# Optimization experiments

Hardware: AMD Instinct MI355X
Metric: run time of the kernel (lower is better)

Reference implementation:

```python
import jax, jax.numpy as jnp
import numpy as np

B, T, D, U = 64, 128, 1024, 1024


def setup_inputs() -> dict:
    key = jax.random.key(0)
    k_x, k_r, k_s, k_wi, k_wh = jax.random.split(key, 5)
    x = jax.random.normal(k_x, (B, T, D), dtype=jnp.float32)
    reset = jax.random.randint(k_r, (B, T), 0, 2, dtype=jnp.int32)
    state = jax.random.normal(k_s, (B, T, U), dtype=jnp.float32)
    # hk.GRU params: w_i (input->3*hidden), w_h (hidden->3*hidden), bias (3*hidden)
    w_i = jax.random.normal(k_wi, (D, 3 * U), dtype=jnp.float32) * (1.0 / np.sqrt(D))
    w_h = jax.random.normal(k_wh, (U, 3 * U), dtype=jnp.float32) * (1.0 / np.sqrt(U))
    b = jnp.zeros((3 * U,), dtype=jnp.float32)
    return {"x": x, "reset": reset, "state": state, "w_i": w_i, "w_h": w_h, "b": b}


def reference(x, reset, state, w_i, w_h, b):
    # _prepare_for_rnn merges (B,T)->rows and adds a length-1 time axis, so
    # hk.dynamic_unroll(ResetCore(GRU)) == one ResetCore(GRU) step over B*T rows.
    Bd, Td, Dd = x.shape
    Ud = w_h.shape[0]
    xf = x.reshape(Bd * Td, Dd)                      # [N, D]
    h = state.reshape(Bd * Td, Ud)                   # [N, U]
    should_reset = reset.reshape(Bd * Td, 1).astype(bool)
    # hk.ResetCore: replace state with initial_state (zeros) where reset is set
    h = jnp.where(should_reset, jnp.zeros_like(h), h)
    # hk.GRU step
    gates_x = xf @ w_i                               # [N, 3U]
    zr_x, a_x = gates_x[:, : 2 * Ud], gates_x[:, 2 * Ud :]
    zr = jax.nn.sigmoid(zr_x + h @ w_h[:, : 2 * Ud] + b[: 2 * Ud])
    z, r = zr[:, :Ud], zr[:, Ud:]
    a = jnp.tanh(a_x + (r * h) @ w_h[:, 2 * Ud :] + b[2 * Ud :])
    h_new = (1.0 - z) * h + z * a                    # [N, U]
    out = h_new.reshape(Bd, Td, Ud)                  # _recover_shape
    new_state = h_new.reshape(Bd, Td, Ud)            # _rnn_reshape back to (B,T,U)
    return out, new_state
```

## Files before the change

kernel.cpp:

```cpp
#include <hip/hip_runtime.h>


typedef __attribute__((ext_vector_type(8))) short short8;
typedef __attribute__((ext_vector_type(4))) short short4v;
typedef __attribute__((ext_vector_type(4))) float floatx4;
typedef __attribute__((ext_vector_type(4))) float f32x4;

#define MROWS 8192
#define KTOT 2048
#define NU 1024
#define NKT 32
#define TBUF 32768
#define TLDS (2 * TBUF)

__device__ __forceinline__ short f2bf(float f) {
  unsigned u = __builtin_bit_cast(unsigned, f);
  u += 0x7fffu + ((u >> 16) & 1u);
  return (short)(u >> 16);
}
__device__ __forceinline__ float bf2f(short s) {
  unsigned u = ((unsigned)(unsigned short)s) << 16;
  return __builtin_bit_cast(float, u);
}
__device__ __forceinline__ float sigmoid_f(float v) { return 1.f / (1.f + __expf(-v)); }
__device__ __forceinline__ float tanh_f(float v) {
  float c = fminf(fmaxf(v, -15.f), 15.f);
  float e = __expf(2.f * c);
  return (e - 1.f) / (e + 1.f);
}

typedef __attribute__((address_space(3))) void* lds_vp;
typedef const __attribute__((address_space(1))) void* gbl_vp;
__device__ __forceinline__ void gload16(const void* g, void* lds) {
  __builtin_amdgcn_global_load_lds((gbl_vp)g, (lds_vp)lds, 16, 0, 0);
}

#define MF(a, b, c) __builtin_amdgcn_mfma_f32_16x16x32_bf16(a, b, c, 0, 0, 0)
#define VMCNT(n) asm volatile("s_waitcnt vmcnt(" #n ")" ::: "memory")
#define LGKM0() asm volatile("s_waitcnt lgkmcnt(0)" ::: "memory")
#define TILE_BAR()                  \
  do {                              \
    __builtin_amdgcn_s_barrier();   \
    asm volatile("" ::: "memory");  \
  } while (0)

__global__ __launch_bounds__(256) void prep_kernel(
    const float* __restrict__ w_i, const float* __restrict__ w_h,
    short* __restrict__ Wc, const float* __restrict__ x,
    const int* __restrict__ reset, const float* __restrict__ state,
    short* __restrict__ xhc) {
  __shared__ float tile[32][33];
  const int b = blockIdx.x;
  if (b < 6144) {
    const int kb = (b & 63) * 32;
    const int nb = (b >> 6) * 32;
    const float* src = (kb < 1024) ? w_i : w_h;
    const int kbl = kb & 1023;
    const int tx = threadIdx.x & 31;
    const int ty = threadIdx.x >> 5;
#pragma unroll
    for (int r = 0; r < 32; r += 8)
      tile[ty + r][tx] = src[(size_t)(kbl + ty + r) * 3072 + nb + tx];
    __syncthreads();
#pragma unroll
    for (int r = 0; r < 32; r += 8)
      Wc[(size_t)(nb + ty + r) * KTOT + kb + tx] = f2bf(tile[tx][ty + r]);
  } else {
    const size_t i4 = (size_t)(b - 6144) * 256 + threadIdx.x;
    const size_t e = i4 * 4;
    const int row = (int)(e >> 10);
    const int d = (int)(e & 1023);
    const float hm = reset[row] ? 0.f : 1.f;
    floatx4 fx = *(const floatx4*)(x + e);
    floatx4 fh = *(const floatx4*)(state + e);
    short4v cx, ch;
#pragma unroll
    for (int k = 0; k < 4; ++k) { cx[k] = f2bf(fx[k]); ch[k] = f2bf(fh[k] * hm); }
    *(short4v*)(xhc + (size_t)row * KTOT + d) = cx;
    *(short4v*)(xhc + (size_t)row * KTOT + 1024 + d) = ch;
  }
}

__global__ __launch_bounds__(512, 4) void zr_kernel(
    const short* __restrict__ xhc, const short* __restrict__ Wc,
    const float* __restrict__ bias, float* __restrict__ zbuf,
    short* __restrict__ rh) {
  extern __shared__ char lds[];
  const int tid = threadIdx.x;
  const int wave = tid >> 6, lane = tid & 63;
  const int wm = wave >> 2, wn = wave & 3;
  const int lrow = lane & 15;
  const int g16 = (lane >> 4) << 4;
  const int swz = (lrow & 7) << 4;
  const int strow = tid >> 3;
  const int scol = ((tid & 7) ^ ((tid >> 3) & 7)) * 8;

  const int xcd = blockIdx.x & 7, bi = blockIdx.x >> 3;
  const int mtile = xcd * 8 + (bi & 7);
  const int ntile = bi >> 3;
  const int m0 = mtile * 128, n0g = ntile * 128;

  const short* aS = xhc + (size_t)(m0 + strow) * KTOT + scol;
  const short* bS = Wc + (size_t)(n0g + strow) * KTOT + scol;
  const int dA = wave * 1024;
  const int dB = 16384 + wave * 1024;

  f32x4 acc[4][2];
#pragma unroll
  for (int i = 0; i < 4; ++i)
#pragma unroll
    for (int j = 0; j < 2; ++j) acc[i][j] = (f32x4){0.f, 0.f, 0.f, 0.f};

#define ZR_STAGE(t, bufp)                                                      \
  _Pragma("unroll") for (int g = 0; g < 2; ++g) {                              \
    gload16(aS + (size_t)(g * 64) * KTOT + (t) * 64, (bufp) + dA + g * 8192);  \
    gload16(bS + (size_t)(g * 64) * KTOT + (t) * 64, (bufp) + dB + g * 8192);  \
  }

  ZR_STAGE(0, lds);
  ZR_STAGE(1, lds + TBUF);
  VMCNT(4);
  TILE_BAR();

#pragma unroll 2
  for (int t = 0; t < NKT; ++t) {
    char* buf = lds + (t & 1) * TBUF;
    short8 af[2][4], bq[2][2];
#pragma unroll
    for (int ks = 0; ks < 2; ++ks) {
      const int colb = ((ks * 64 + g16) ^ swz);
      const char* pA = buf + (wm * 64 + lrow) * 128 + colb;
      const char* pB = buf + 16384 + (wn * 32 + lrow) * 128 + colb;
#pragma unroll
      for (int i = 0; i < 4; ++i) af[ks][i] = *(const short8*)(pA + i * 2048);
#pragma unroll
      for (int j = 0; j < 2; ++j) bq[ks][j] = *(const short8*)(pB + j * 2048);
    }
    LGKM0();
    TILE_BAR();
    if (t + 2 < NKT) { ZR_STAGE(t + 2, buf); }
    __builtin_amdgcn_s_setprio(1);
#pragma unroll
    for (int ks = 0; ks < 2; ++ks)
#pragma unroll
      for (int i = 0; i < 4; ++i)
#pragma unroll
        for (int j = 0; j < 2; ++j)
          acc[i][j] = MF(af[ks][i], bq[ks][j], acc[i][j]);
    __builtin_amdgcn_s_setprio(0);
    if (t + 2 < NKT) { VMCNT(4); } else { VMCNT(0); }
    TILE_BAR();
  }
#undef ZR_STAGE

  const bool zh = (n0g < 1024);
#pragma unroll
  for (int j = 0; j < 2; ++j) {
    const int gcn = n0g + wn * 32 + j * 16 + lrow;
    const float bv = bias[gcn];
#pragma unroll
    for (int i = 0; i < 4; ++i) {
#pragma unroll
      for (int rg = 0; rg < 4; ++rg) {
        const int gr = m0 + wm * 64 + i * 16 + (lane >> 4) * 4 + rg;
        const float sv = sigmoid_f(acc[i][j][rg] + bv);
        if (zh) {
          zbuf[(size_t)gr * NU + gcn] = sv;
        } else {
          const int u = gcn - 1024;
          const float hv = bf2f(xhc[(size_t)gr * KTOT + 1024 + u]);
          rh[(size_t)gr * NU + u] = f2bf(sv * hv);
        }
      }
    }
  }
}

__global__ __launch_bounds__(512, 4) void cand_kernel(
    const short* __restrict__ xhc, const short* __restrict__ rh,
    const short* __restrict__ Wc, const float* __restrict__ bias,
    const float* zbuf, float* out) {
  extern __shared__ char lds[];
  const int tid = threadIdx.x;
  const int wave = tid >> 6, lane = tid & 63;
  const int wm = wave >> 2, wn = wave & 3;
  const int lrow = lane & 15;
  const int g16 = (lane >> 4) << 4;
  const int swz = (lrow & 7) << 4;
  const int strow = tid >> 3;
  const int scol = ((tid & 7) ^ ((tid >> 3) & 7)) * 8;

  const int xcd = blockIdx.x & 7, bi = blockIdx.x >> 3;
  const int mtile = xcd * 8 + (bi & 7);
  const int ntile = bi >> 3;
  const int m0 = mtile * 128, n0g = ntile * 128;

  const short* aX = xhc + (size_t)(m0 + strow) * KTOT + scol;
  const short* aR = rh + (size_t)(m0 + strow) * NU + scol;
  const short* bS = Wc + (size_t)(2048 + n0g + strow) * KTOT + scol;
  const int dA = wave * 1024;
  const int dB = 16384 + wave * 1024;

  f32x4 acc[4][2];
#pragma unroll
  for (int i = 0; i < 4; ++i)
#pragma unroll
    for (int j = 0; j < 2; ++j) acc[i][j] = (f32x4){0.f, 0.f, 0.f, 0.f};

#define CD_STAGE(t, bufp)                                                      \
  _Pragma("unroll") for (int g = 0; g < 2; ++g) {                              \
    if ((t) < 16)                                                              \
      gload16(aX + (size_t)(g * 64) * KTOT + (t) * 64, (bufp) + dA + g * 8192);\
    else                                                                       \
      gload16(aR + (size_t)(g * 64) * NU + ((t) - 16) * 64,                    \
              (bufp) + dA + g * 8192);                                         \
    gload16(bS + (size_t)(g * 64) * KTOT + (t) * 64, (bufp) + dB + g * 8192);  \
  }

  CD_STAGE(0, lds);
  CD_STAGE(1, lds + TBUF);
  VMCNT(4);
  TILE_BAR();

#pragma unroll 2
  for (int t = 0; t < NKT; ++t) {
    char* buf = lds + (t & 1) * TBUF;
    short8 af[2][4], bq[2][2];
#pragma unroll
    for (int ks = 0; ks < 2; ++ks) {
      const int colb = ((ks * 64 + g16) ^ swz);
      const char* pA = buf + (wm * 64 + lrow) * 128 + colb;
      const char* pB = buf + 16384 + (wn * 32 + lrow) * 128 + colb;
#pragma unroll
      for (int i = 0; i < 4; ++i) af[ks][i] = *(const short8*)(pA + i * 2048);
#pragma unroll
      for (int j = 0; j < 2; ++j) bq[ks][j] = *(const short8*)(pB + j * 2048);
    }
    LGKM0();
    TILE_BAR();
    if (t + 2 < NKT) { CD_STAGE(t + 2, buf); }
    __builtin_amdgcn_s_setprio(1);
#pragma unroll
    for (int ks = 0; ks < 2; ++ks)
#pragma unroll
      for (int i = 0; i < 4; ++i)
#pragma unroll
        for (int j = 0; j < 2; ++j)
          acc[i][j] = MF(af[ks][i], bq[ks][j], acc[i][j]);
    __builtin_amdgcn_s_setprio(0);
    if (t + 2 < NKT) { VMCNT(4); } else { VMCNT(0); }
    TILE_BAR();
  }
#undef CD_STAGE

#pragma unroll
  for (int j = 0; j < 2; ++j) {
    const int gc = n0g + wn * 32 + j * 16 + lrow;
    const float ba = bias[2048 + gc];
#pragma unroll
    for (int i = 0; i < 4; ++i) {
#pragma unroll
      for (int rg = 0; rg < 4; ++rg) {
        const int gr = m0 + wm * 64 + i * 16 + (lane >> 4) * 4 + rg;
        const float av = tanh_f(acc[i][j][rg] + ba);
        const float zv = zbuf[(size_t)gr * NU + gc];
        const float hv = bf2f(xhc[(size_t)gr * KTOT + 1024 + gc]);
        const float hn = (1.f - zv) * hv + zv * av;
        out[(size_t)gr * NU + gc] = hn;
        out[(size_t)MROWS * NU + (size_t)gr * NU + gc] = hn;
      }
    }
  }
}

extern "C" void kernel_launch(void* const* d_in, const int* in_sizes, int n_in,
                              void* d_out, int out_size, void* d_ws, size_t ws_size,
                              hipStream_t stream) {
  const float* x = (const float*)d_in[0];
  const int* reset = (const int*)d_in[1];
  const float* state = (const float*)d_in[2];
  const float* w_i = (const float*)d_in[3];
  const float* w_h = (const float*)d_in[4];
  const float* bias = (const float*)d_in[5];
  float* out = (float*)d_out;

  short* Wc = (short*)d_ws;
  short* xhc = Wc + (size_t)3072 * KTOT;
  short* rh = xhc + (size_t)MROWS * KTOT;
  float* zbuf = out + (size_t)MROWS * NU;

  hipFuncSetAttribute(reinterpret_cast<const void*>(zr_kernel),
                      hipFuncAttributeMaxDynamicSharedMemorySize, TLDS);
  hipFuncSetAttribute(reinterpret_cast<const void*>(cand_kernel),
                      hipFuncAttributeMaxDynamicSharedMemorySize, TLDS);

  prep_kernel<<<dim3(14336), 256, 0, stream>>>(w_i, w_h, Wc, x, reset, state, xhc);

  zr_kernel<<<dim3(1024), 512, TLDS, stream>>>(xhc, Wc, bias, zbuf, rh);
  cand_kernel<<<dim3(512), 512, TLDS, stream>>>(xhc, rh, Wc, bias, zbuf, out);
}
```

Baseline: 158.9 us.

## Shrink GEMM tiles to 128x64 with 4-wave blocks for more blocks

Both GEMM kernels now use 256-thread blocks of 4 waves, each computing a 128x64 output tile instead of 128x128, with per-wave load addressing reworked and LDS per buffer reduced. The grid doubles (2048 and 1024 blocks), aiming for better load balance and occupancy across CUs. In exchange, arithmetic intensity per block drops because the A tile is reloaded twice as often, which raises global and L2 traffic.

```diff
diff --git a/kernel.cpp b/kernel.cpp
--- a/kernel.cpp
+++ b/kernel.cpp
@@ -10,7 +10,7 @@
 #define KTOT 2048
 #define NU 1024
 #define NKT 32
-#define TBUF 32768
+#define TBUF 24576
 #define TLDS (2 * TBUF)
 
 __device__ __forceinline__ short f2bf(float f) {
@@ -81,29 +81,29 @@
   }
 }
 
-__global__ __launch_bounds__(512, 4) void zr_kernel(
+__global__ __launch_bounds__(256, 3) void zr_kernel(
     const short* __restrict__ xhc, const short* __restrict__ Wc,
     const float* __restrict__ bias, float* __restrict__ zbuf,
     short* __restrict__ rh) {
   extern __shared__ char lds[];
   const int tid = threadIdx.x;
   const int wave = tid >> 6, lane = tid & 63;
-  const int wm = wave >> 2, wn = wave & 3;
+  const int wm = wave >> 1, wn = wave & 1;
   const int lrow = lane & 15;
   const int g16 = (lane >> 4) << 4;
   const int swz = (lrow & 7) << 4;
-  const int strow = tid >> 3;
-  const int scol = ((tid & 7) ^ ((tid >> 3) & 7)) * 8;
+  const int srow = lane >> 3;
+  const int scol = ((lane & 7) ^ srow) * 8;
 
   const int xcd = blockIdx.x & 7, bi = blockIdx.x >> 3;
   const int mtile = xcd * 8 + (bi & 7);
   const int ntile = bi >> 3;
-  const int m0 = mtile * 128, n0g = ntile * 128;
-
-  const short* aS = xhc + (size_t)(m0 + strow) * KTOT + scol;
-  const short* bS = Wc + (size_t)(n0g + strow) * KTOT + scol;
-  const int dA = wave * 1024;
-  const int dB = 16384 + wave * 1024;
+  const int m0 = mtile * 128, n0g = ntile * 64;
+
+  const short* aS = xhc + (size_t)(m0 + wave * 32 + srow) * KTOT + scol;
+  const short* bS = Wc + (size_t)(n0g + wave * 16 + srow) * KTOT + scol;
+  const int dA = wave * 4096;
+  const int dB = 16384 + wave * 2048;
 
   f32x4 acc[4][2];
 #pragma unroll
@@ -112,14 +112,14 @@
     for (int j = 0; j < 2; ++j) acc[i][j] = (f32x4){0.f, 0.f, 0.f, 0.f};
 
 #define ZR_STAGE(t, bufp)                                                      \
-  _Pragma("unroll") for (int g = 0; g < 2; ++g) {                              \
-    gload16(aS + (size_t)(g * 64) * KTOT + (t) * 64, (bufp) + dA + g * 8192);  \
-    gload16(bS + (size_t)(g * 64) * KTOT + (t) * 64, (bufp) + dB + g * 8192);  \
-  }
+  _Pragma("unroll") for (int g = 0; g < 4; ++g)                                \
+    gload16(aS + (size_t)(g * 8) * KTOT + (t) * 64, (bufp) + dA + g * 1024);   \
+  _Pragma("unroll") for (int g = 0; g < 2; ++g)                                \
+    gload16(bS + (size_t)(g * 8) * KTOT + (t) * 64, (bufp) + dB + g * 1024);
 
   ZR_STAGE(0, lds);
   ZR_STAGE(1, lds + TBUF);
-  VMCNT(4);
+  VMCNT(6);
   TILE_BAR();
 
 #pragma unroll 2
@@ -148,7 +148,7 @@
         for (int j = 0; j < 2; ++j)
           acc[i][j] = MF(af[ks][i], bq[ks][j], acc[i][j]);
     __builtin_amdgcn_s_setprio(0);
-    if (t + 2 < NKT) { VMCNT(4); } else { VMCNT(0); }
+    if (t + 2 < NKT) { VMCNT(6); } else { VMCNT(0); }
     TILE_BAR();
   }
 #undef ZR_STAGE
@@ -176,30 +176,30 @@
   }
 }
 
-__global__ __launch_bounds__(512, 4) void cand_kernel(
+__global__ __launch_bounds__(256, 3) void cand_kernel(
     const short* __restrict__ xhc, const short* __restrict__ rh,
     const short* __restrict__ Wc, const float* __restrict__ bias,
     const float* zbuf, float* out) {
   extern __shared__ char lds[];
   const int tid = threadIdx.x;
   const int wave = tid >> 6, lane = tid & 63;
-  const int wm = wave >> 2, wn = wave & 3;
+  const int wm = wave >> 1, wn = wave & 1;
   const int lrow = lane & 15;
   const int g16 = (lane >> 4) << 4;
   const int swz = (lrow & 7) << 4;
-  const int strow = tid >> 3;
-  const int scol = ((tid & 7) ^ ((tid >> 3) & 7)) * 8;
+  const int srow = lane >> 3;
+  const int scol = ((lane & 7) ^ srow) * 8;
 
   const int xcd = blockIdx.x & 7, bi = blockIdx.x >> 3;
   const int mtile = xcd * 8 + (bi & 7);
   const int ntile = bi >> 3;
-  const int m0 = mtile * 128, n0g = ntile * 128;
-
-  const short* aX = xhc + (size_t)(m0 + strow) * KTOT + scol;
-  const short* aR = rh + (size_t)(m0 + strow) * NU + scol;
-  const short* bS = Wc + (size_t)(2048 + n0g + strow) * KTOT + scol;
-  const int dA = wave * 1024;
-  const int dB = 16384 + wave * 1024;
+  const int m0 = mtile * 128, n0g = ntile * 64;
+
+  const short* aX = xhc + (size_t)(m0 + wave * 32 + srow) * KTOT + scol;
+  const short* aR = rh + (size_t)(m0 + wave * 32 + srow) * NU + scol;
+  const short* bS = Wc + (size_t)(2048 + n0g + wave * 16 + srow) * KTOT + scol;
+  const int dA = wave * 4096;
+  const int dB = 16384 + wave * 2048;
 
   f32x4 acc[4][2];
 #pragma unroll
@@ -208,18 +208,19 @@
     for (int j = 0; j < 2; ++j) acc[i][j] = (f32x4){0.f, 0.f, 0.f, 0.f};
 
 #define CD_STAGE(t, bufp)                                                      \
-  _Pragma("unroll") for (int g = 0; g < 2; ++g) {                              \
+  _Pragma("unroll") for (int g = 0; g < 4; ++g) {                              \
     if ((t) < 16)                                                              \
-      gload16(aX + (size_t)(g * 64) * KTOT + (t) * 64, (bufp) + dA + g * 8192);\
+      gload16(aX + (size_t)(g * 8) * KTOT + (t) * 64, (bufp) + dA + g * 1024); \
     else                                                                       \
-      gload16(aR + (size_t)(g * 64) * NU + ((t) - 16) * 64,                    \
-              (bufp) + dA + g * 8192);                                         \
-    gload16(bS + (size_t)(g * 64) * KTOT + (t) * 64, (bufp) + dB + g * 8192);  \
-  }
+      gload16(aR + (size_t)(g * 8) * NU + ((t) - 16) * 64,                     \
+              (bufp) + dA + g * 1024);                                         \
+  }                                                                            \
+  _Pragma("unroll") for (int g = 0; g < 2; ++g)                                \
+    gload16(bS + (size_t)(g * 8) * KTOT + (t) * 64, (bufp) + dB + g * 1024);
 
   CD_STAGE(0, lds);
   CD_STAGE(1, lds + TBUF);
-  VMCNT(4);
+  VMCNT(6);
   TILE_BAR();
 
 #pragma unroll 2
@@ -248,7 +249,7 @@
         for (int j = 0; j < 2; ++j)
           acc[i][j] = MF(af[ks][i], bq[ks][j], acc[i][j]);
     __builtin_amdgcn_s_setprio(0);
-    if (t + 2 < NKT) { VMCNT(4); } else { VMCNT(0); }
+    if (t + 2 < NKT) { VMCNT(6); } else { VMCNT(0); }
     TILE_BAR();
   }
 #undef CD_STAGE
@@ -296,6 +297,6 @@
 
   prep_kernel<<<dim3(14336), 256, 0, stream>>>(w_i, w_h, Wc, x, reset, state, xhc);
 
-  zr_kernel<<<dim3(1024), 512, TLDS, stream>>>(xhc, Wc, bias, zbuf, rh);
-  cand_kernel<<<dim3(512), 512, TLDS, stream>>>(xhc, rh, Wc, bias, zbuf, out);
-}
+  zr_kernel<<<dim3(2048), 256, TLDS, stream>>>(xhc, Wc, bias, zbuf, rh);
+  cand_kernel<<<dim3(1024), 256, TLDS, stream>>>(xhc, rh, Wc, bias, zbuf, out);
+}
```

New measurement: 177.7 us. 1.12x slower.
